# Kernel optimization log

Hardware: AMD Instinct MI355X
Metric: run time of the kernel (lower is better)

## Reference

```python
import jax, jax.numpy as jnp
import numpy as np

IO, H, S, N = 64, 1024, 512, 64

def setup_inputs() -> dict:
    key = jax.random.key(0)
    ks = jax.random.split(key, 6)
    scale = 0.05  # keep activations in a sane range for tanh/softmax
    return {
        "states": jax.random.normal(ks[0], (N, S, H), jnp.float32) * scale,
        "output_set": jax.random.normal(ks[1], (IO, H), jnp.float32) * scale,
        "Wo": jax.random.normal(ks[2], (2 * H, H), jnp.float32) * scale,
        "bo": jax.random.normal(ks[3], (H,), jnp.float32) * scale,
        "Wc": jax.random.normal(ks[4], (IO * H, IO), jnp.float32) * scale,
        "bc": jax.random.normal(ks[5], (IO,), jnp.float32) * scale,
    }

def reference(states, output_set, Wo, bo, Wc, bc):
    # Batched over the n_states Python loop of the original module.
    # attn scores: output_set [io,h] x states [n,s,h] -> [n,io,s]
    attn = jnp.einsum('ih,nsh->nis', output_set, states)
    attn = jax.nn.softmax(attn, axis=-1)  # softmax over context (sm_over_context=True)
    mix = jnp.einsum('nis,nsh->nih', attn, states)            # [n,io,h]
    out = jnp.broadcast_to(output_set[None], mix.shape)       # [n,io,h]
    combined = jnp.concatenate([mix, out], axis=-1)           # [n,io,2h]
    o = combined @ Wo + bo                                    # linear_out: 2h -> h
    logits = jnp.tanh(o).reshape(o.shape[0], -1) @ Wc + bc    # C: io*h -> io
    return logits
```

## Files before the change

kernel.cpp:

```cpp
#include <hip/hip_runtime.h>
#include <hip/hip_bf16.h>

#define IOdim 64
#define Hdim  1024
#define Sdim  512
#define Nbat  64

typedef __bf16 bf16x8_t __attribute__((ext_vector_type(8)));
typedef float  f32x4_t  __attribute__((ext_vector_type(4)));

#define MFMA16(a, b, c) __builtin_amdgcn_mfma_f32_16x16x32_bf16((a), (b), (c), 0, 0, 0)

__device__ __forceinline__ unsigned short f2bf(float f) {
    return __builtin_bit_cast(unsigned short, (__bf16)f);
}
__device__ __forceinline__ bf16x8_t cvt8(float4 p0, float4 p1) {
    bf16x8_t b;
    b[0] = (__bf16)p0.x; b[1] = (__bf16)p0.y; b[2] = (__bf16)p0.z; b[3] = (__bf16)p0.w;
    b[4] = (__bf16)p1.x; b[5] = (__bf16)p1.y; b[6] = (__bf16)p1.z; b[7] = (__bf16)p1.w;
    return b;
}
__device__ __forceinline__ void async16(const void* g, void* l) {
    __builtin_amdgcn_global_load_lds(
        (const __attribute__((address_space(1))) void*)g,
        (__attribute__((address_space(3))) void*)l, 16, 0, 0);
}
#define PIPE_SYNC() do { \
    asm volatile("s_waitcnt vmcnt(0)" ::: "memory"); \
    __builtin_amdgcn_s_barrier(); \
} while (0)

__global__ __launch_bounds__(256) void cvt_kernel(const float* __restrict__ in,
                                                  unsigned short* __restrict__ outp,
                                                  int nElem) {
    int idx = blockIdx.x * 256 + threadIdx.x;
    if (idx < nElem) outp[idx] = f2bf(in[idx]);
}

__global__ __launch_bounds__(256) void transpose_cvt(const float* __restrict__ in,
                                                     unsigned short* __restrict__ outp,
                                                     int R, int C) {
    __shared__ float tile[32][33];
    int c0 = blockIdx.x * 32, r0 = blockIdx.y * 32;
    int tx = threadIdx.x, ty = threadIdx.y;
#pragma unroll
    for (int i = 0; i < 4; i++) {
        int r = ty + i * 8;
        tile[r][tx] = in[(size_t)(r0 + r) * C + c0 + tx];
    }
    __syncthreads();
#pragma unroll
    for (int i = 0; i < 4; i++) {
        int r = ty + i * 8;
        outp[(size_t)(c0 + r) * R + r0 + tx] = f2bf(tile[tx][r]);
    }
}

__global__ __launch_bounds__(256) void ob_kernel(const unsigned short* __restrict__ osb,
                                                 const unsigned short* __restrict__ woT,
                                                 const float* __restrict__ bo,
                                                 float* __restrict__ ob) {
    int h0 = blockIdx.x * 64;
    int tid = threadIdx.x, lane = tid & 63, w = tid >> 6;
    int col = lane & 15, quad = lane >> 4;
    f32x4_t acc[4] = {};
    const unsigned short* bp  = woT + (size_t)(h0 + w * 16 + col) * 2048 + 1024 + quad * 8;
    const unsigned short* apb = osb + (size_t)col * 1024 + quad * 8;
    for (int kc = 0; kc < 1024; kc += 32) {
        bf16x8_t bfrag = *(const bf16x8_t*)(bp + kc);
#pragma unroll
        for (int a = 0; a < 4; a++) {
            bf16x8_t afrag = *(const bf16x8_t*)(apb + (size_t)a * 16 * 1024 + kc);
            acc[a] = MFMA16(bfrag, afrag, acc[a]);
        }
    }
#pragma unroll
    for (int a = 0; a < 4; a++)
#pragma unroll
        for (int r = 0; r < 4; r++) {
            int i = a * 16 + col;
            int h = h0 + w * 16 + quad * 4 + r;
            ob[(size_t)i * Hdim + h] = acc[a][r] + bo[h];
        }
}

__global__ __launch_bounds__(256) void scores_kernel(const float* __restrict__ states,
                                                     const unsigned short* __restrict__ osb,
                                                     float* __restrict__ attnf) {
    __shared__ float Bst[2][64 * 64];
    __shared__ unsigned short Ast[2][64 * 64];
    int n = blockIdx.y, s0 = blockIdx.x * 64;
    int tid = threadIdx.x, lane = tid & 63, w = tid >> 6;
    int col = lane & 15, quad = lane >> 4;
    const float* bsrc = states + ((size_t)(n * Sdim + s0 + (tid >> 4)) << 10)
                      + (((tid & 15) ^ ((tid >> 4) & 7)) << 2);
    const unsigned short* asrc = osb + ((size_t)(tid >> 3) << 10)
                      + (((tid & 7) ^ ((tid >> 3) & 7)) << 3);
    int xs = col & 7;
    int R = w * 16 + col;
    float* B0 = Bst[0]; float* B1 = Bst[1];
    unsigned short* A0 = Ast[0]; unsigned short* A1 = Ast[1];
    f32x4_t acc[4] = {};

#define SC_STAGE(kc, Bb, Ab) do { \
    _Pragma("unroll") for (int j = 0; j < 4; j++) \
        async16(bsrc + ((size_t)j << 14) + (kc), (Bb) + tid * 4 + j * 1024); \
    _Pragma("unroll") for (int j = 0; j < 2; j++) \
        async16(asrc + ((size_t)j << 15) + (kc), (Ab) + tid * 8 + j * 2048); \
} while (0)

    SC_STAGE(0, B0, A0);
    PIPE_SYNC();
    for (int t = 0; t < 16; ++t) {
        if (t + 1 < 16) SC_STAGE((t + 1) * 64, B1, A1);
#pragma unroll
        for (int kk = 0; kk < 2; kk++) {
            int sg = kk * 8 + quad * 2;
            float4 f0 = *(const float4*)(B0 + R * 64 + ((sg ^ xs) << 2));
            float4 f1 = *(const float4*)(B0 + R * 64 + (((sg + 1) ^ xs) << 2));
            bf16x8_t bfrag = cvt8(f0, f1);
#pragma unroll
            for (int a = 0; a < 4; a++) {
                bf16x8_t afrag = *(const bf16x8_t*)(A0 + (a * 16 + col) * 64
                                                    + (((kk * 4 + quad) ^ xs) << 3));
                acc[a] = MFMA16(afrag, bfrag, acc[a]);
            }
        }
        PIPE_SYNC();
        float* tB = B0; B0 = B1; B1 = tB;
        unsigned short* tA = A0; A0 = A1; A1 = tA;
    }
#undef SC_STAGE
    float* obp = attnf + (size_t)(n * IOdim) * Sdim + s0 + w * 16 + col;
#pragma unroll
    for (int a = 0; a < 4; a++)
#pragma unroll
        for (int r = 0; r < 4; r++) {
            int i = a * 16 + quad * 4 + r;
            obp[(size_t)i * Sdim] = acc[a][r];
        }
}

__global__ __launch_bounds__(256) void softmax_kernel(const float* __restrict__ attnf,
                                                      unsigned short* __restrict__ attnb) {
    int row = blockIdx.x * 4 + (threadIdx.x >> 6);
    int lane = threadIdx.x & 63;
    const float* p = attnf + (size_t)row * Sdim + lane * 8;
    float4 v0 = ((const float4*)p)[0];
    float4 v1 = ((const float4*)p)[1];
    float v[8] = {v0.x, v0.y, v0.z, v0.w, v1.x, v1.y, v1.z, v1.w};
    float m = v[0];
#pragma unroll
    for (int j = 1; j < 8; j++) m = fmaxf(m, v[j]);
#pragma unroll
    for (int off = 32; off > 0; off >>= 1) m = fmaxf(m, __shfl_xor(m, off));
    float sum = 0.f;
#pragma unroll
    for (int j = 0; j < 8; j++) { v[j] = __expf(v[j] - m); sum += v[j]; }
#pragma unroll
    for (int off = 32; off > 0; off >>= 1) sum += __shfl_xor(sum, off);
    float inv = 1.0f / sum;
    union { unsigned short u[8]; uint4 q; } res;
#pragma unroll
    for (int j = 0; j < 8; j++) res.u[j] = f2bf(v[j] * inv);
    *(uint4*)(attnb + (size_t)row * Sdim + lane * 8) = res.q;
}

__global__ __launch_bounds__(256) void mix_kernel(const float* __restrict__ states,
                                                  const unsigned short* __restrict__ attnb,
                                                  unsigned short* __restrict__ mixb) {
    __shared__ unsigned short Tlds[2][64 * 72];
    int n = blockIdx.y, h0 = blockIdx.x * 64;
    int tid = threadIdx.x, lane = tid & 63, g = tid >> 6;
    int col = lane & 15, quad = lane >> 4;
    f32x4_t acc0 = {0,0,0,0}, acc1 = {0,0,0,0}, acc2 = {0,0,0,0}, acc3 = {0,0,0,0};
    const unsigned short* ap = attnb + (size_t)(n * IOdim + col) * Sdim + quad * 8;
    const float* sbase = states + (size_t)n * Sdim * Hdim + h0 + lane;
    float cur[16];
#pragma unroll
    for (int rep = 0; rep < 16; rep++) cur[rep] = sbase[(size_t)(g * 16 + rep) * Hdim];
    for (int t = 0; t < 8; ++t) {
        int sc = t * 64;
        unsigned short* Tb = Tlds[t & 1];
        union { unsigned short u[16]; uint4 q[2]; } pk;
#pragma unroll
        for (int rep = 0; rep < 16; rep++) pk.u[rep] = f2bf(cur[rep]);
        *(uint4*)(Tb + lane * 72 + g * 16)     = pk.q[0];
        *(uint4*)(Tb + lane * 72 + g * 16 + 8) = pk.q[1];
        if (t + 1 < 8) {
#pragma unroll
            for (int rep = 0; rep < 16; rep++)
                cur[rep] = sbase[(size_t)(sc + 64 + g * 16 + rep) * Hdim];
        }
        __syncthreads();
#pragma unroll
        for (int ks = 0; ks < 64; ks += 32) {
            bf16x8_t b  = *(const bf16x8_t*)(Tb + (g * 16 + col) * 72 + ks + quad * 8);
            bf16x8_t a0 = *(const bf16x8_t*)(ap + sc + ks);
            bf16x8_t a1 = *(const bf16x8_t*)(ap + 16 * Sdim + sc + ks);
            bf16x8_t a2 = *(const bf16x8_t*)(ap + 32 * Sdim + sc + ks);
            bf16x8_t a3 = *(const bf16x8_t*)(ap + 48 * Sdim + sc + ks);
            acc0 = MFMA16(a0, b, acc0);
            acc1 = MFMA16(a1, b, acc1);
            acc2 = MFMA16(a2, b, acc2);
            acc3 = MFMA16(a3, b, acc3);
        }
    }
    f32x4_t accs[4] = {acc0, acc1, acc2, acc3};
    int h = h0 + g * 16 + col;
#pragma unroll
    for (int ai = 0; ai < 4; ai++)
#pragma unroll
        for (int r = 0; r < 4; r++) {
            int i = ai * 16 + quad * 4 + r;
            mixb[(size_t)(n * IOdim + i) * Hdim + h] = f2bf(accs[ai][r]);
        }
}

__global__ __launch_bounds__(256) void out_gemm(const unsigned short* __restrict__ mixb,
                                                const unsigned short* __restrict__ woT,
                                                const float* __restrict__ ob,
                                                unsigned short* __restrict__ tb) {
    __shared__ unsigned short Ald[2][128 * 64];
    __shared__ unsigned short Bld[2][64 * 64];
    int h0 = blockIdx.x * 64, r0 = blockIdx.y * 128;
    int tid = threadIdx.x, lane = tid & 63, w = tid >> 6;
    int col = lane & 15, quad = lane >> 4;
    int wx = w & 1, wy = w >> 1;
    int sw = ((tid & 7) ^ ((tid >> 3) & 7)) * 8;
    const unsigned short* m1 = mixb + (size_t)(r0 + (tid >> 3)) * Hdim + sw;
    const unsigned short* w1 = woT + (size_t)(h0 + (tid >> 3)) * 2048 + sw;
    int xs = col & 7;
    unsigned short* A0 = Ald[0]; unsigned short* A1 = Ald[1];
    unsigned short* B0 = Bld[0]; unsigned short* B1 = Bld[1];
    f32x4_t acc[4][2] = {};

#define OG_STAGE(kc, Ab, Bb) do { \
    _Pragma("unroll") for (int j = 0; j < 4; j++) \
        async16(m1 + (size_t)j * 32 * Hdim + (kc), (Ab) + tid * 8 + j * 2048); \
    _Pragma("unroll") for (int j = 0; j < 2; j++) \
        async16(w1 + (size_t)j * 32 * 2048 + (kc), (Bb) + tid * 8 + j * 2048); \
} while (0)

    OG_STAGE(0, A0, B0);
    PIPE_SYNC();
    for (int t = 0; t < 16; ++t) {
        if (t + 1 < 16) OG_STAGE((t + 1) * 64, A1, B1);
#pragma unroll
        for (int kk = 0; kk < 2; kk++) {
            bf16x8_t bfr[2];
#pragma unroll
            for (int ni = 0; ni < 2; ni++)
                bfr[ni] = *(const bf16x8_t*)(B0 + (wx * 32 + ni * 16 + col) * 64
                                             + (((kk * 4 + quad) ^ xs) << 3));
#pragma unroll
            for (int mi = 0; mi < 4; mi++) {
                bf16x8_t af = *(const bf16x8_t*)(A0 + (wy * 64 + mi * 16 + col) * 64
                                                 + (((kk * 4 + quad) ^ xs) << 3));
#pragma unroll
                for (int ni = 0; ni < 2; ni++)
                    acc[mi][ni] = MFMA16(af, bfr[ni], acc[mi][ni]);
            }
        }
        PIPE_SYNC();
        unsigned short* tp;
        tp = A0; A0 = A1; A1 = tp;
        tp = B0; B0 = B1; B1 = tp;
    }
#undef OG_STAGE
#pragma unroll
    for (int ni = 0; ni < 2; ni++) {
        int h = h0 + wx * 32 + ni * 16 + col;
#pragma unroll
        for (int mi = 0; mi < 4; mi++)
#pragma unroll
            for (int r = 0; r < 4; r++) {
                int rr = r0 + wy * 64 + mi * 16 + quad * 4 + r;
                int i = rr & 63;
                tb[(size_t)rr * Hdim + h] = f2bf(tanhf(acc[mi][ni][r] + ob[(size_t)i * Hdim + h]));
            }
    }
}

__global__ __launch_bounds__(256) void final_gemm(const unsigned short* __restrict__ tb,
                                                  const unsigned short* __restrict__ wcT,
                                                  float* __restrict__ partials) {
    int kc0 = blockIdx.x * 128;
    int tid = threadIdx.x, lane = tid & 63, g = tid >> 6;
    int col = lane & 15, quad = lane >> 4;
    f32x4_t acc0 = {0,0,0,0}, acc1 = {0,0,0,0}, acc2 = {0,0,0,0}, acc3 = {0,0,0,0};
    const unsigned short* ap = tb + (size_t)col * 65536 + kc0 + quad * 8;
    const unsigned short* bp = wcT + (size_t)(g * 16 + col) * 65536 + kc0 + quad * 8;
    bf16x8_t B[2], A0[2], A1[2], A2[2], A3[2];
#pragma unroll
    for (int t = 0; t < 2; t++) {
        B[t]  = *(const bf16x8_t*)(bp + t * 32);
        A0[t] = *(const bf16x8_t*)(ap + t * 32);
        A1[t] = *(const bf16x8_t*)(ap + (size_t)16 * 65536 + t * 32);
        A2[t] = *(const bf16x8_t*)(ap + (size_t)32 * 65536 + t * 32);
        A3[t] = *(const bf16x8_t*)(ap + (size_t)48 * 65536 + t * 32);
    }
#pragma unroll
    for (int c = 0; c < 4; c++) {
        int p = c & 1;
        acc0 = MFMA16(A0[p], B[p], acc0);
        acc1 = MFMA16(A1[p], B[p], acc1);
        acc2 = MFMA16(A2[p], B[p], acc2);
        acc3 = MFMA16(A3[p], B[p], acc3);
        if (c + 2 < 4) {
            int kn = (c + 2) * 32;
            B[p]  = *(const bf16x8_t*)(bp + kn);
            A0[p] = *(const bf16x8_t*)(ap + kn);
            A1[p] = *(const bf16x8_t*)(ap + (size_t)16 * 65536 + kn);
            A2[p] = *(const bf16x8_t*)(ap + (size_t)32 * 65536 + kn);
            A3[p] = *(const bf16x8_t*)(ap + (size_t)48 * 65536 + kn);
        }
    }
    f32x4_t accs[4] = {acc0, acc1, acc2, acc3};
    int j = g * 16 + col;
    float* pb = partials + blockIdx.x * 4096;
#pragma unroll
    for (int ai = 0; ai < 4; ai++)
#pragma unroll
        for (int r = 0; r < 4; r++) {
            int nn = ai * 16 + quad * 4 + r;
            pb[nn * 64 + j] = accs[ai][r];
        }
}

__global__ __launch_bounds__(256) void reduce_kernel(const float* __restrict__ partials,
                                                     const float* __restrict__ bc,
                                                     float* __restrict__ out) {
    __shared__ float red[4][64];
    int tid = threadIdx.x, lane = tid & 63, w = tid >> 6;
    int idx = blockIdx.x * 64 + lane;
    float s = 0.f;
#pragma unroll 4
    for (int c = w; c < 512; c += 4) s += partials[(size_t)c * 4096 + idx];
    red[w][lane] = s;
    __syncthreads();
    if (w == 0)
        out[idx] = red[0][lane] + red[1][lane] + red[2][lane] + red[3][lane] + bc[idx & 63];
}

extern "C" void kernel_launch(void* const* d_in, const int* in_sizes, int n_in,
                              void* d_out, int out_size, void* d_ws, size_t ws_size,
                              hipStream_t stream) {
    const float* states     = (const float*)d_in[0];
    const float* output_set = (const float*)d_in[1];
    const float* Wo         = (const float*)d_in[2];
    const float* bo         = (const float*)d_in[3];
    const float* Wc         = (const float*)d_in[4];
    const float* bc         = (const float*)d_in[5];
    float* out = (float*)d_out;

    char* ws = (char*)d_ws;
    float*          attnf = (float*)ws;
    float*          parts = (float*)ws;
    unsigned short* attnb = (unsigned short*)(ws + (8u  << 20));
    unsigned short* mixb  = (unsigned short*)(ws + (12u << 20));
    unsigned short* tb    = (unsigned short*)(ws + (20u << 20));
    unsigned short* woT   = (unsigned short*)(ws + (28u << 20));
    unsigned short* osb   = (unsigned short*)(ws + (32u << 20));
    unsigned short* wcT   = (unsigned short*)(ws + (32u << 20) + (1u << 18));
    float*          obuf  = (float*)(ws + (40u << 20) + (1u << 18));

    cvt_kernel<<<dim3(IOdim * Hdim / 256), dim3(256), 0, stream>>>(output_set, osb, IOdim * Hdim);
    transpose_cvt<<<dim3(Hdim / 32, 2048 / 32), dim3(32, 8), 0, stream>>>(Wo, woT, 2048, Hdim);
    transpose_cvt<<<dim3(64 / 32, 65536 / 32), dim3(32, 8), 0, stream>>>(Wc, wcT, 65536, 64);
    ob_kernel<<<dim3(Hdim / 64), dim3(256), 0, stream>>>(osb, woT, bo, obuf);
    scores_kernel<<<dim3(Sdim / 64, Nbat), dim3(256), 0, stream>>>(states, osb, attnf);
    softmax_kernel<<<dim3(Nbat * IOdim / 4), dim3(256), 0, stream>>>(attnf, attnb);
    mix_kernel<<<dim3(Hdim / 64, Nbat), dim3(256), 0, stream>>>(states, attnb, mixb);
    out_gemm<<<dim3(Hdim / 64, Nbat * IOdim / 128), dim3(256), 0, stream>>>(mixb, woT, obuf, tb);
    final_gemm<<<dim3(512), dim3(256), 0, stream>>>(tb, wcT, parts);
    reduce_kernel<<<dim3(64), dim3(256), 0, stream>>>(parts, bc, out);
}
```

Measured before the change: 327.5 us.

## Retile scores and final GEMM kernels around single-shot swizzled LDS slabs

```diff
diff --git a/kernel.cpp b/kernel.cpp
--- a/kernel.cpp
+++ b/kernel.cpp
@@ -87,58 +87,35 @@
 __global__ __launch_bounds__(256) void scores_kernel(const float* __restrict__ states,
                                                      const unsigned short* __restrict__ osb,
                                                      float* __restrict__ attnf) {
-    __shared__ float Bst[2][64 * 64];
-    __shared__ unsigned short Ast[2][64 * 64];
-    int n = blockIdx.y, s0 = blockIdx.x * 64;
-    int tid = threadIdx.x, lane = tid & 63, w = tid >> 6;
-    int col = lane & 15, quad = lane >> 4;
-    const float* bsrc = states + ((size_t)(n * Sdim + s0 + (tid >> 4)) << 10)
-                      + (((tid & 15) ^ ((tid >> 4) & 7)) << 2);
-    const unsigned short* asrc = osb + ((size_t)(tid >> 3) << 10)
-                      + (((tid & 7) ^ ((tid >> 3) & 7)) << 3);
-    int xs = col & 7;
-    int R = w * 16 + col;
-    float* B0 = Bst[0]; float* B1 = Bst[1];
-    unsigned short* A0 = Ast[0]; unsigned short* A1 = Ast[1];
-    f32x4_t acc[4] = {};
-
-#define SC_STAGE(kc, Bb, Ab) do { \
-    _Pragma("unroll") for (int j = 0; j < 4; j++) \
-        async16(bsrc + ((size_t)j << 14) + (kc), (Bb) + tid * 4 + j * 1024); \
-    _Pragma("unroll") for (int j = 0; j < 2; j++) \
-        async16(asrc + ((size_t)j << 15) + (kc), (Ab) + tid * 8 + j * 2048); \
-} while (0)
-
-    SC_STAGE(0, B0, A0);
+    __shared__ float slab[16 * 1024];
+    int n = blockIdx.y, s0 = blockIdx.x * 16;
+    int tid = threadIdx.x, lane = tid & 63, w = tid >> 6;
+    int col = lane & 15, quad = lane >> 4;
+    const float* base = states + ((size_t)(n * Sdim + s0) << 10);
+#pragma unroll
+    for (int j = 0; j < 16; j++) {
+        int swz = (tid & ~15) | ((tid ^ j) & 15);
+        async16(base + ((size_t)j << 10) + (swz << 2), slab + j * 1024 + tid * 4);
+    }
     PIPE_SYNC();
-    for (int t = 0; t < 16; ++t) {
-        if (t + 1 < 16) SC_STAGE((t + 1) * 64, B1, A1);
-#pragma unroll
-        for (int kk = 0; kk < 2; kk++) {
-            int sg = kk * 8 + quad * 2;
-            float4 f0 = *(const float4*)(B0 + R * 64 + ((sg ^ xs) << 2));
-            float4 f1 = *(const float4*)(B0 + R * 64 + (((sg + 1) ^ xs) << 2));
-            bf16x8_t bfrag = cvt8(f0, f1);
-#pragma unroll
-            for (int a = 0; a < 4; a++) {
-                bf16x8_t afrag = *(const bf16x8_t*)(A0 + (a * 16 + col) * 64
-                                                    + (((kk * 4 + quad) ^ xs) << 3));
-                acc[a] = MFMA16(afrag, bfrag, acc[a]);
-            }
-        }
-        PIPE_SYNC();
-        float* tB = B0; B0 = B1; B1 = tB;
-        unsigned short* tA = A0; A0 = A1; A1 = tA;
-    }
-#undef SC_STAGE
-    float* obp = attnf + (size_t)(n * IOdim) * Sdim + s0 + w * 16 + col;
-#pragma unroll
-    for (int a = 0; a < 4; a++)
-#pragma unroll
-        for (int r = 0; r < 4; r++) {
-            int i = a * 16 + quad * 4 + r;
-            obp[(size_t)i * Sdim] = acc[a][r];
-        }
+    const unsigned short* ap = osb + (size_t)(w * 16 + col) * 1024 + quad * 8;
+    const float* brow = slab + col * 1024;
+    f32x4_t acc = {0, 0, 0, 0};
+#pragma unroll 8
+    for (int ks = 0; ks < 32; ks++) {
+        int sg0 = ks * 8 + quad * 2;
+        int p0 = (sg0 & ~15) | ((sg0 ^ col) & 15);
+        int p1 = ((sg0 + 1) & ~15) | (((sg0 + 1) ^ col) & 15);
+        float4 f0 = *(const float4*)(brow + (p0 << 2));
+        float4 f1 = *(const float4*)(brow + (p1 << 2));
+        bf16x8_t bfrag = cvt8(f0, f1);
+        bf16x8_t afrag = *(const bf16x8_t*)(ap + ks * 32);
+        acc = MFMA16(afrag, bfrag, acc);
+    }
+    float* obp = attnf + (size_t)(n * IOdim + w * 16 + quad * 4) * Sdim + s0 + col;
+#pragma unroll
+    for (int r = 0; r < 4; r++)
+        obp[(size_t)r * Sdim] = acc[r];
 }
 
 __global__ __launch_bounds__(256) void softmax_kernel(const float* __restrict__ attnf,
@@ -285,46 +262,42 @@
 __global__ __launch_bounds__(256) void final_gemm(const unsigned short* __restrict__ tb,
                                                   const unsigned short* __restrict__ wcT,
                                                   float* __restrict__ partials) {
-    int kc0 = blockIdx.x * 128;
-    int tid = threadIdx.x, lane = tid & 63, g = tid >> 6;
-    int col = lane & 15, quad = lane >> 4;
-    f32x4_t acc0 = {0,0,0,0}, acc1 = {0,0,0,0}, acc2 = {0,0,0,0}, acc3 = {0,0,0,0};
-    const unsigned short* ap = tb + (size_t)col * 65536 + kc0 + quad * 8;
-    const unsigned short* bp = wcT + (size_t)(g * 16 + col) * 65536 + kc0 + quad * 8;
-    bf16x8_t B[2], A0[2], A1[2], A2[2], A3[2];
-#pragma unroll
-    for (int t = 0; t < 2; t++) {
-        B[t]  = *(const bf16x8_t*)(bp + t * 32);
-        A0[t] = *(const bf16x8_t*)(ap + t * 32);
-        A1[t] = *(const bf16x8_t*)(ap + (size_t)16 * 65536 + t * 32);
-        A2[t] = *(const bf16x8_t*)(ap + (size_t)32 * 65536 + t * 32);
-        A3[t] = *(const bf16x8_t*)(ap + (size_t)48 * 65536 + t * 32);
-    }
-#pragma unroll
-    for (int c = 0; c < 4; c++) {
-        int p = c & 1;
-        acc0 = MFMA16(A0[p], B[p], acc0);
-        acc1 = MFMA16(A1[p], B[p], acc1);
-        acc2 = MFMA16(A2[p], B[p], acc2);
-        acc3 = MFMA16(A3[p], B[p], acc3);
-        if (c + 2 < 4) {
-            int kn = (c + 2) * 32;
-            B[p]  = *(const bf16x8_t*)(bp + kn);
-            A0[p] = *(const bf16x8_t*)(ap + kn);
-            A1[p] = *(const bf16x8_t*)(ap + (size_t)16 * 65536 + kn);
-            A2[p] = *(const bf16x8_t*)(ap + (size_t)32 * 65536 + kn);
-            A3[p] = *(const bf16x8_t*)(ap + (size_t)48 * 65536 + kn);
-        }
-    }
-    f32x4_t accs[4] = {acc0, acc1, acc2, acc3};
-    int j = g * 16 + col;
-    float* pb = partials + blockIdx.x * 4096;
-#pragma unroll
-    for (int ai = 0; ai < 4; ai++)
+    __shared__ unsigned short Atile[64 * 256];
+    __shared__ unsigned short Btile[64 * 256];
+    size_t kb0 = (size_t)blockIdx.x * 512;
+    int tid = threadIdx.x, lane = tid & 63, w = tid >> 6;
+    int col = lane & 15, quad = lane >> 4;
+#pragma unroll
+    for (int c = 0; c < 8; c++) {
+        int lin = c * 256 + tid;
+        int row = lin >> 5, cs = lin & 31;
+        int swz = (cs & ~15) | ((cs ^ row) & 15);
+        const char* asrc = (const char*)tb  + (size_t)row * 131072 + kb0 + swz * 16;
+        const char* bsrc = (const char*)wcT + (size_t)row * 131072 + kb0 + swz * 16;
+        async16(asrc, (char*)Atile + lin * 16);
+        async16(bsrc, (char*)Btile + lin * 16);
+    }
+    PIPE_SYNC();
+    f32x4_t acc[4] = {};
+#pragma unroll
+    for (int ks = 0; ks < 8; ks++) {
+        int sg = ks * 4 + quad;
+        int ph = (sg & ~15) | ((sg ^ col) & 15);
+        bf16x8_t bf = *(const bf16x8_t*)(Btile + (w * 16 + col) * 256 + ph * 8);
+#pragma unroll
+        for (int a = 0; a < 4; a++) {
+            bf16x8_t af = *(const bf16x8_t*)(Atile + (a * 16 + col) * 256 + ph * 8);
+            acc[a] = MFMA16(af, bf, acc[a]);
+        }
+    }
+    float* pb = partials + (size_t)blockIdx.x * 4096;
+    int j = w * 16 + col;
+#pragma unroll
+    for (int a = 0; a < 4; a++)
 #pragma unroll
         for (int r = 0; r < 4; r++) {
-            int nn = ai * 16 + quad * 4 + r;
-            pb[nn * 64 + j] = accs[ai][r];
+            int nn = a * 16 + quad * 4 + r;
+            pb[nn * 64 + j] = acc[a][r];
         }
 }
 
@@ -336,7 +309,7 @@
     int idx = blockIdx.x * 64 + lane;
     float s = 0.f;
 #pragma unroll 4
-    for (int c = w; c < 512; c += 4) s += partials[(size_t)c * 4096 + idx];
+    for (int c = w; c < 256; c += 4) s += partials[(size_t)c * 4096 + idx];
     red[w][lane] = s;
     __syncthreads();
     if (w == 0)
@@ -369,10 +342,10 @@
     transpose_cvt<<<dim3(Hdim / 32, 2048 / 32), dim3(32, 8), 0, stream>>>(Wo, woT, 2048, Hdim);
     transpose_cvt<<<dim3(64 / 32, 65536 / 32), dim3(32, 8), 0, stream>>>(Wc, wcT, 65536, 64);
     ob_kernel<<<dim3(Hdim / 64), dim3(256), 0, stream>>>(osb, woT, bo, obuf);
-    scores_kernel<<<dim3(Sdim / 64, Nbat), dim3(256), 0, stream>>>(states, osb, attnf);
+    scores_kernel<<<dim3(Sdim / 16, Nbat), dim3(256), 0, stream>>>(states, osb, attnf);
     softmax_kernel<<<dim3(Nbat * IOdim / 4), dim3(256), 0, stream>>>(attnf, attnb);
     mix_kernel<<<dim3(Hdim / 64, Nbat), dim3(256), 0, stream>>>(states, attnb, mixb);
     out_gemm<<<dim3(Hdim / 64, Nbat * IOdim / 128), dim3(256), 0, stream>>>(mixb, woT, obuf, tb);
-    final_gemm<<<dim3(512), dim3(256), 0, stream>>>(tb, wcT, parts);
+    final_gemm<<<dim3(256), dim3(256), 0, stream>>>(tb, wcT, parts);
     reduce_kernel<<<dim3(64), dim3(256), 0, stream>>>(parts, bc, out);
 }
```

New measurement: 332.8 us. About the same (+1.6%).
